# Kernel tuning notes

Measured on AMD Instinct MI355X. Metric: run time of the kernel, lower is better.

## Reference

```python
import jax, jax.numpy as jnp
import numpy as np

D = 1024
H = 16


def setup_inputs() -> dict:
    key = jax.random.key(0)
    ks = jax.random.split(key, 5)
    s = 1.0 / np.sqrt(D)
    x = jax.random.normal(ks[0], (4, 1024, D), dtype=jnp.float32)
    W_qkv = jax.random.normal(ks[1], (D, 3 * D), dtype=jnp.float32) * s
    b_qkv = jnp.zeros((3 * D,), dtype=jnp.float32)
    W_out = jax.random.normal(ks[2], (D, D), dtype=jnp.float32) * s
    b_out = jnp.zeros((D,), dtype=jnp.float32)
    return {"x": x, "W_qkv": W_qkv, "b_qkv": b_qkv, "W_out": W_out, "b_out": b_out}


def reference(x, W_qkv, b_qkv, W_out, b_out):
    bs, ns, d = x.shape
    dh = d // H
    scale = 1.0 / np.sqrt(dh)
    qkv = x @ W_qkv + b_qkv                      # [B,S,3D]
    qkv = qkv.reshape(bs, ns, 3, H, dh)
    q, k, v = qkv[:, :, 0], qkv[:, :, 1], qkv[:, :, 2]  # [B,S,H,dh]
    # attention scores [B,H,S,S]
    attn = jnp.einsum('bqhd,bkhd->bhqk', q, k) * scale
    attn = jax.nn.softmax(attn, axis=-1)
    out = jnp.einsum('bhqk,bkhd->bqhd', attn, v)  # [B,S,H,dh]
    out = out.reshape(bs, ns, d)
    return out @ W_out + b_out
```

## Files before the change

### kernel.cpp

```cpp
#include <hip/hip_runtime.h>
#include <hip/hip_bf16.h>
#include <cstdint>

typedef __bf16 bf16x8 __attribute__((ext_vector_type(8)));
typedef float f32x4 __attribute__((ext_vector_type(4)));

__device__ __forceinline__ unsigned short f2b(float f) {
  __bf16 h = (__bf16)f;
  return __builtin_bit_cast(unsigned short, h);
}

__device__ __forceinline__ void gload_lds16(const void* g, void* l) {
  __builtin_amdgcn_global_load_lds(
      (__attribute__((address_space(1))) void*)g,
      (__attribute__((address_space(3))) void*)l,
      16, 0, 0);
}

__global__ void cvt_f32_bf16(const float* __restrict__ in,
                             unsigned short* __restrict__ out, int n) {
  int i = (blockIdx.x * blockDim.x + threadIdx.x) * 4;
  if (i + 3 < n) {
    float4 f = *(const float4*)&in[i];
    ushort4 u = make_ushort4(f2b(f.x), f2b(f.y), f2b(f.z), f2b(f.w));
    *(ushort4*)&out[i] = u;
  }
}

__global__ void transpose_cvt(const float* __restrict__ in,
                              unsigned short* __restrict__ out, int R, int C) {
  __shared__ float tile[32][33];
  int c0 = blockIdx.x * 32, r0 = blockIdx.y * 32;
  int x = threadIdx.x, y = threadIdx.y;
  #pragma unroll
  for (int j = y; j < 32; j += 8)
    tile[j][x] = in[(size_t)(r0 + j) * C + c0 + x];
  __syncthreads();
  #pragma unroll
  for (int j = y; j < 32; j += 8)
    out[(size_t)(c0 + j) * R + r0 + x] = f2b(tile[x][j]);
}

__global__ void transpose_v(const unsigned short* __restrict__ qkv,
                            unsigned short* __restrict__ vt) {
  __shared__ unsigned short tile[32][33];
  int bh = blockIdx.x, s0 = blockIdx.y * 32, d0 = blockIdx.z * 32;
  int b = bh >> 4, h = bh & 15;
  int x = threadIdx.x, y = threadIdx.y;
  #pragma unroll
  for (int j = y; j < 32; j += 8)
    tile[j][x] = qkv[(size_t)(b * 1024 + s0 + j) * 3072 + 2048 + h * 64 + d0 + x];
  __syncthreads();
  #pragma unroll
  for (int j = y; j < 32; j += 8)
    vt[(size_t)(bh * 64 + d0 + j) * 1024 + s0 + x] = tile[x][j];
}

template <int OUT_F32>
__global__ __launch_bounds__(256, 2)
void gemm_bt(const unsigned short* __restrict__ A,
             const unsigned short* __restrict__ Bt,
             const float* __restrict__ bias, void* __restrict__ C,
             int M, int N, int K) {
  __shared__ __align__(16) unsigned short sA[128 * 32];
  __shared__ __align__(16) unsigned short sB[128 * 32];
  const int t = threadIdx.x;
  const int w = t >> 6, lane = t & 63;
  const int ln = lane & 15, lq = lane >> 4;
  const int wr = w >> 1, wc = w & 1;
  const int m0 = blockIdx.y * 128, n0 = blockIdx.x * 128;

  f32x4 acc[4][4];
  #pragma unroll
  for (int i = 0; i < 4; i++)
    #pragma unroll
    for (int j = 0; j < 4; j++) acc[i][j] = (f32x4){0.f, 0.f, 0.f, 0.f};

  for (int k0 = 0; k0 < K; k0 += 32) {
    __syncthreads();
    #pragma unroll
    for (int i = 0; i < 2; ++i) {
      int idx = i * 256 + t;
      int row = idx >> 2;
      int cb = (idx & 3) * 8;
      gload_lds16(A + (size_t)(m0 + row) * K + k0 + cb, &sA[idx * 8]);
    }
    #pragma unroll
    for (int i = 0; i < 2; ++i) {
      int idx = i * 256 + t;
      int row = idx >> 2;
      int cb = (idx & 3) * 8;
      gload_lds16(Bt + (size_t)(n0 + row) * K + k0 + cb, &sB[idx * 8]);
    }
    __syncthreads();
    bf16x8 af[4], bfr[4];
    #pragma unroll
    for (int m = 0; m < 4; m++)
      af[m] = *(const bf16x8*)&sA[(wr * 64 + m * 16 + ln) * 32 + lq * 8];
    #pragma unroll
    for (int n = 0; n < 4; n++)
      bfr[n] = *(const bf16x8*)&sB[(wc * 64 + n * 16 + ln) * 32 + lq * 8];
    #pragma unroll
    for (int m = 0; m < 4; m++)
      #pragma unroll
      for (int n = 0; n < 4; n++)
        acc[m][n] = __builtin_amdgcn_mfma_f32_16x16x32_bf16(af[m], bfr[n], acc[m][n], 0, 0, 0);
  }

  #pragma unroll
  for (int m = 0; m < 4; m++) {
    #pragma unroll
    for (int n = 0; n < 4; n++) {
      int col = n0 + wc * 64 + n * 16 + ln;
      float bv = bias[col];
      #pragma unroll
      for (int r = 0; r < 4; r++) {
        int row = m0 + wr * 64 + m * 16 + lq * 4 + r;
        float v = acc[m][n][r] + bv;
        if (OUT_F32)
          ((float*)C)[(size_t)row * N + col] = v;
        else
          ((unsigned short*)C)[(size_t)row * N + col] = f2b(v);
      }
    }
  }
}

__global__ __launch_bounds__(256, 4)
void attn_fwd(const unsigned short* __restrict__ qkv,
              const unsigned short* __restrict__ vt,
              unsigned short* __restrict__ aout) {
  const int b = blockIdx.z, h = blockIdx.y, q0 = blockIdx.x * 64;
  __shared__ __align__(16) unsigned short sB[4][64 * 64];
  __shared__ __align__(16) unsigned short sP[4][16 * 64];
  const int t = threadIdx.x;
  const int w = t >> 6, lane = t & 63;
  const int ln = lane & 15, lq = lane >> 4;
  const float SCALE = 0.125f;

  const size_t qbase = (size_t)(b * 1024 + q0) * 3072 + h * 64;
  const size_t kbase = (size_t)(b * 1024) * 3072 + 1024 + h * 64;
  const size_t vbase = (size_t)((b * 16 + h) * 64) * 1024;

  #pragma unroll
  for (int i = 0; i < 2; i++) {
    int idx = i * 256 + t;
    int row = idx >> 3, ch = idx & 7;
    int sw = (ch ^ (row & 7)) * 8;
    gload_lds16(qkv + qbase + (size_t)row * 3072 + sw, &sB[0][idx * 8]);
    gload_lds16(qkv + kbase + (size_t)row * 3072 + sw, &sB[1][idx * 8]);
    gload_lds16(vt + vbase + (size_t)row * 1024 + sw, &sB[2][idx * 8]);
  }
  __syncthreads();
  bf16x8 qf[2];
  #pragma unroll
  for (int c = 0; c < 2; c++) {
    int row = w * 16 + ln;
    qf[c] = *(const bf16x8*)&sB[0][row * 64 + ((c * 4 + lq) ^ (ln & 7)) * 8];
  }
  __syncthreads();

  f32x4 o[4];
  float mrow = -1e30f, lsum = 0.f;
  #pragma unroll
  for (int n = 0; n < 4; n++) o[n] = (f32x4){0.f, 0.f, 0.f, 0.f};

  for (int kt = 0; kt < 16; ++kt) {
    const unsigned short* kb = sB[(kt & 1) ? 3 : 1];
    const unsigned short* vb = sB[(kt & 1) ? 0 : 2];
    if (kt < 15) {
      const int kv1 = (kt + 1) * 64;
      unsigned short* kn = sB[(kt & 1) ? 1 : 3];
      unsigned short* vn = sB[(kt & 1) ? 2 : 0];
      #pragma unroll
      for (int i = 0; i < 2; i++) {
        int idx = i * 256 + t;
        int row = idx >> 3, ch = idx & 7;
        int sw = (ch ^ (row & 7)) * 8;
        gload_lds16(qkv + kbase + (size_t)(kv1 + row) * 3072 + sw, &kn[idx * 8]);
        gload_lds16(vt + vbase + (size_t)row * 1024 + kv1 + sw, &vn[idx * 8]);
      }
    }

    f32x4 st[4];
    #pragma unroll
    for (int kc = 0; kc < 4; kc++) st[kc] = (f32x4){0.f, 0.f, 0.f, 0.f};
    #pragma unroll
    for (int kc = 0; kc < 4; kc++) {
      int krow = kc * 16 + ln;
      bf16x8 k0f = *(const bf16x8*)&kb[krow * 64 + ((0 + lq) ^ (ln & 7)) * 8];
      bf16x8 k1f = *(const bf16x8*)&kb[krow * 64 + ((4 + lq) ^ (ln & 7)) * 8];
      st[kc] = __builtin_amdgcn_mfma_f32_16x16x32_bf16(k0f, qf[0], st[kc], 0, 0, 0);
      st[kc] = __builtin_amdgcn_mfma_f32_16x16x32_bf16(k1f, qf[1], st[kc], 0, 0, 0);
    }

    float xv[4][4];
    float tm = -1e30f;
    #pragma unroll
    for (int kc = 0; kc < 4; kc++) {
      #pragma unroll
      for (int r = 0; r < 4; r++) {
        xv[kc][r] = st[kc][r] * SCALE;
        tm = fmaxf(tm, xv[kc][r]);
      }
    }
    tm = fmaxf(tm, __shfl_xor(tm, 16));
    tm = fmaxf(tm, __shfl_xor(tm, 32));
    float mn = fmaxf(mrow, tm);
    float al = __expf(mrow - mn);
    mrow = mn;
    float ts = 0.f;
    #pragma unroll
    for (int kc = 0; kc < 4; kc++) {
      #pragma unroll
      for (int r = 0; r < 4; r++) {
        xv[kc][r] = __expf(xv[kc][r] - mn);
        ts += xv[kc][r];
      }
    }
    ts += __shfl_xor(ts, 16);
    ts += __shfl_xor(ts, 32);
    lsum = lsum * al + ts;

    #pragma unroll
    for (int r = 0; r < 4; r++) {
      float alr = __shfl(al, (lane & 48) | (lq * 4 + r));
      #pragma unroll
      for (int n = 0; n < 4; n++) o[n][r] *= alr;
    }

    unsigned char* pb = (unsigned char*)sP[w];
    #pragma unroll
    for (int kc = 0; kc < 4; kc++) {
      ushort4 u = make_ushort4(f2b(xv[kc][0]), f2b(xv[kc][1]),
                               f2b(xv[kc][2]), f2b(xv[kc][3]));
      int boff = (kc * 32 + lq * 8) ^ ((ln & 7) << 4);
      *(ushort4*)(pb + ln * 128 + boff) = u;
    }

    #pragma unroll
    for (int c2 = 0; c2 < 2; c2++) {
      bf16x8 pa = *(const bf16x8*)&sP[w][ln * 64 + ((c2 * 4 + lq) ^ (ln & 7)) * 8];
      #pragma unroll
      for (int n = 0; n < 4; n++) {
        int vrow = n * 16 + ln;
        bf16x8 vf = *(const bf16x8*)&vb[vrow * 64 + ((c2 * 4 + lq) ^ (ln & 7)) * 8];
        o[n] = __builtin_amdgcn_mfma_f32_16x16x32_bf16(pa, vf, o[n], 0, 0, 0);
      }
    }

    asm volatile("s_waitcnt vmcnt(0)" ::: "memory");
    __builtin_amdgcn_s_barrier();
  }

  float linv[4];
  #pragma unroll
  for (int r = 0; r < 4; r++)
    linv[r] = 1.f / __shfl(lsum, (lane & 48) | (lq * 4 + r));
  #pragma unroll
  for (int n = 0; n < 4; n++) {
    #pragma unroll
    for (int r = 0; r < 4; r++) {
      int row = q0 + w * 16 + lq * 4 + r;
      int col = h * 64 + n * 16 + ln;
      aout[(size_t)(b * 1024 + row) * 1024 + col] = f2b(o[n][r] * linv[r]);
    }
  }
}

extern "C" void kernel_launch(void* const* d_in, const int* in_sizes, int n_in,
                              void* d_out, int out_size, void* d_ws, size_t ws_size,
                              hipStream_t stream) {
  const float* x = (const float*)d_in[0];
  const float* W_qkv = (const float*)d_in[1];
  const float* b_qkv = (const float*)d_in[2];
  const float* W_out = (const float*)d_in[3];
  const float* b_out = (const float*)d_in[4];
  float* out = (float*)d_out;

  char* ws = (char*)d_ws;
  unsigned short* xb    = (unsigned short*)(ws);
  unsigned short* wqkvT = (unsigned short*)(ws + 8388608);
  unsigned short* woutT = (unsigned short*)(ws + 14680064);
  unsigned short* qkv   = (unsigned short*)(ws + 16777216);
  unsigned short* vt    = (unsigned short*)(ws + 41943040);
  unsigned short* aout  = (unsigned short*)(ws + 50331648);
  if (ws_size < 58720256) return;

  cvt_f32_bf16<<<4096, 256, 0, stream>>>(x, xb, 4096 * 1024);
  transpose_cvt<<<dim3(96, 32), dim3(32, 8), 0, stream>>>(W_qkv, wqkvT, 1024, 3072);
  transpose_cvt<<<dim3(32, 32), dim3(32, 8), 0, stream>>>(W_out, woutT, 1024, 1024);
  gemm_bt<0><<<dim3(24, 32), 256, 0, stream>>>(xb, wqkvT, b_qkv, qkv, 4096, 3072, 1024);
  transpose_v<<<dim3(64, 32, 2), dim3(32, 8), 0, stream>>>(qkv, vt);
  attn_fwd<<<dim3(16, 16, 4), 256, 0, stream>>>(qkv, vt, aout);
  gemm_bt<1><<<dim3(8, 32), 256, 0, stream>>>(aout, woutT, b_out, out, 4096, 1024, 1024);
}
```

Before: 125.2 us.

## Load K/V fragments directly from global, add lazy softmax rescale with exp2

The attention kernel no longer stages Q, K and V through double-buffered LDS with global_load_lds and block barriers. Each wave now reads its MFMA fragments straight from global memory, relying on L2 for reuse across the four waves. The softmax moves to exp2 with a folded scale and only rescales the running max and accumulators when some row's max grows past a threshold. MFMA sections are wrapped in s_setprio. This removes barriers and LDS traffic, but adds uncoalesced, unpipelined global loads with no prefetch, so each wave stalls on memory latency every tile.

```diff
diff --git a/kernel.cpp b/kernel.cpp
--- a/kernel.cpp
+++ b/kernel.cpp
@@ -131,34 +131,21 @@
               const unsigned short* __restrict__ vt,
               unsigned short* __restrict__ aout) {
   const int b = blockIdx.z, h = blockIdx.y, q0 = blockIdx.x * 64;
-  __shared__ __align__(16) unsigned short sB[4][64 * 64];
   __shared__ __align__(16) unsigned short sP[4][16 * 64];
   const int t = threadIdx.x;
   const int w = t >> 6, lane = t & 63;
   const int ln = lane & 15, lq = lane >> 4;
-  const float SCALE = 0.125f;
-
-  const size_t qbase = (size_t)(b * 1024 + q0) * 3072 + h * 64;
-  const size_t kbase = (size_t)(b * 1024) * 3072 + 1024 + h * 64;
-  const size_t vbase = (size_t)((b * 16 + h) * 64) * 1024;
-
-  #pragma unroll
-  for (int i = 0; i < 2; i++) {
-    int idx = i * 256 + t;
-    int row = idx >> 3, ch = idx & 7;
-    int sw = (ch ^ (row & 7)) * 8;
-    gload_lds16(qkv + qbase + (size_t)row * 3072 + sw, &sB[0][idx * 8]);
-    gload_lds16(qkv + kbase + (size_t)row * 3072 + sw, &sB[1][idx * 8]);
-    gload_lds16(vt + vbase + (size_t)row * 1024 + sw, &sB[2][idx * 8]);
-  }
-  __syncthreads();
+  const float K2 = 0.125f * 1.44269504f;
+  const float THR = 11.54f;
+
+  const unsigned short* qp = qkv + (size_t)(b * 1024 + q0 + w * 16) * 3072 + h * 64;
+  const unsigned short* kp = qkv + (size_t)(b * 1024) * 3072 + 1024 + h * 64;
+  const unsigned short* vp = vt + (size_t)((b * 16 + h) * 64) * 1024;
+
   bf16x8 qf[2];
   #pragma unroll
-  for (int c = 0; c < 2; c++) {
-    int row = w * 16 + ln;
-    qf[c] = *(const bf16x8*)&sB[0][row * 64 + ((c * 4 + lq) ^ (ln & 7)) * 8];
-  }
-  __syncthreads();
+  for (int c = 0; c < 2; c++)
+    qf[c] = *(const bf16x8*)&qp[(size_t)ln * 3072 + (c * 4 + lq) * 8];
 
   f32x4 o[4];
   float mrow = -1e30f, lsum = 0.f;
@@ -166,32 +153,25 @@
   for (int n = 0; n < 4; n++) o[n] = (f32x4){0.f, 0.f, 0.f, 0.f};
 
   for (int kt = 0; kt < 16; ++kt) {
-    const unsigned short* kb = sB[(kt & 1) ? 3 : 1];
-    const unsigned short* vb = sB[(kt & 1) ? 0 : 2];
-    if (kt < 15) {
-      const int kv1 = (kt + 1) * 64;
-      unsigned short* kn = sB[(kt & 1) ? 1 : 3];
-      unsigned short* vn = sB[(kt & 1) ? 2 : 0];
-      #pragma unroll
-      for (int i = 0; i < 2; i++) {
-        int idx = i * 256 + t;
-        int row = idx >> 3, ch = idx & 7;
-        int sw = (ch ^ (row & 7)) * 8;
-        gload_lds16(qkv + kbase + (size_t)(kv1 + row) * 3072 + sw, &kn[idx * 8]);
-        gload_lds16(vt + vbase + (size_t)row * 1024 + kv1 + sw, &vn[idx * 8]);
-      }
-    }
+    const int kv0 = kt * 64;
+
+    bf16x8 vf[4][2];
+    #pragma unroll
+    for (int n = 0; n < 4; n++)
+      #pragma unroll
+      for (int c2 = 0; c2 < 2; c2++)
+        vf[n][c2] = *(const bf16x8*)&vp[(size_t)(n * 16 + ln) * 1024 + kv0 + c2 * 32 + lq * 8];
 
     f32x4 st[4];
     #pragma unroll
-    for (int kc = 0; kc < 4; kc++) st[kc] = (f32x4){0.f, 0.f, 0.f, 0.f};
-    #pragma unroll
-    for (int kc = 0; kc < 4; kc++) {
-      int krow = kc * 16 + ln;
-      bf16x8 k0f = *(const bf16x8*)&kb[krow * 64 + ((0 + lq) ^ (ln & 7)) * 8];
-      bf16x8 k1f = *(const bf16x8*)&kb[krow * 64 + ((4 + lq) ^ (ln & 7)) * 8];
-      st[kc] = __builtin_amdgcn_mfma_f32_16x16x32_bf16(k0f, qf[0], st[kc], 0, 0, 0);
+    for (int kc = 0; kc < 4; kc++) {
+      const unsigned short* kr = &kp[(size_t)(kv0 + kc * 16 + ln) * 3072];
+      bf16x8 k0f = *(const bf16x8*)&kr[lq * 8];
+      bf16x8 k1f = *(const bf16x8*)&kr[32 + lq * 8];
+      __builtin_amdgcn_s_setprio(1);
+      st[kc] = __builtin_amdgcn_mfma_f32_16x16x32_bf16(k0f, qf[0], (f32x4){0.f, 0.f, 0.f, 0.f}, 0, 0, 0);
       st[kc] = __builtin_amdgcn_mfma_f32_16x16x32_bf16(k1f, qf[1], st[kc], 0, 0, 0);
+      __builtin_amdgcn_s_setprio(0);
     }
 
     float xv[4][4];
@@ -200,34 +180,38 @@
     for (int kc = 0; kc < 4; kc++) {
       #pragma unroll
       for (int r = 0; r < 4; r++) {
-        xv[kc][r] = st[kc][r] * SCALE;
+        xv[kc][r] = st[kc][r] * K2;
         tm = fmaxf(tm, xv[kc][r]);
       }
     }
     tm = fmaxf(tm, __shfl_xor(tm, 16));
     tm = fmaxf(tm, __shfl_xor(tm, 32));
-    float mn = fmaxf(mrow, tm);
-    float al = __expf(mrow - mn);
-    mrow = mn;
+
+    if (!__all(tm <= mrow + THR)) {
+      float mn = fmaxf(mrow, tm);
+      float al = exp2f(mrow - mn);
+      mrow = mn;
+      lsum *= al;
+      #pragma unroll
+      for (int r = 0; r < 4; r++) {
+        float alr = __shfl(al, (lane & 48) | (lq * 4 + r));
+        #pragma unroll
+        for (int n = 0; n < 4; n++) o[n][r] *= alr;
+      }
+    }
+
     float ts = 0.f;
     #pragma unroll
     for (int kc = 0; kc < 4; kc++) {
       #pragma unroll
       for (int r = 0; r < 4; r++) {
-        xv[kc][r] = __expf(xv[kc][r] - mn);
+        xv[kc][r] = exp2f(xv[kc][r] - mrow);
         ts += xv[kc][r];
       }
     }
     ts += __shfl_xor(ts, 16);
     ts += __shfl_xor(ts, 32);
-    lsum = lsum * al + ts;
-
-    #pragma unroll
-    for (int r = 0; r < 4; r++) {
-      float alr = __shfl(al, (lane & 48) | (lq * 4 + r));
-      #pragma unroll
-      for (int n = 0; n < 4; n++) o[n][r] *= alr;
-    }
+    lsum += ts;
 
     unsigned char* pb = (unsigned char*)sP[w];
     #pragma unroll
@@ -241,16 +225,12 @@
     #pragma unroll
     for (int c2 = 0; c2 < 2; c2++) {
       bf16x8 pa = *(const bf16x8*)&sP[w][ln * 64 + ((c2 * 4 + lq) ^ (ln & 7)) * 8];
-      #pragma unroll
-      for (int n = 0; n < 4; n++) {
-        int vrow = n * 16 + ln;
-        bf16x8 vf = *(const bf16x8*)&vb[vrow * 64 + ((c2 * 4 + lq) ^ (ln & 7)) * 8];
-        o[n] = __builtin_amdgcn_mfma_f32_16x16x32_bf16(pa, vf, o[n], 0, 0, 0);
-      }
-    }
-
-    asm volatile("s_waitcnt vmcnt(0)" ::: "memory");
-    __builtin_amdgcn_s_barrier();
+      __builtin_amdgcn_s_setprio(1);
+      #pragma unroll
+      for (int n = 0; n < 4; n++)
+        o[n] = __builtin_amdgcn_mfma_f32_16x16x32_bf16(pa, vf[n][c2], o[n], 0, 0, 0);
+      __builtin_amdgcn_s_setprio(0);
+    }
   }
 
   float linv[4];
```

Measured after the change: 199.2 us. 59.2% more time.
